# Kernel optimization log

Hardware: AMD Instinct MI355X
Metric: run time of the kernel (lower is better)

The kernel has to match this reference:

```python
import jax, jax.numpy as jnp
import numpy as np

N_VOXELS = 128
N_PARAMS = 8
N_QUERIES = 4194304


def setup_inputs() -> dict:
    key = jax.random.key(0)
    k1, k2 = jax.random.split(key)
    ipos = jax.random.uniform(k1, (N_QUERIES, 3), dtype=jnp.float32)  # positions in [0,1]^3
    grid = 0.01 * jax.random.normal(k2, (N_VOXELS, N_VOXELS, N_VOXELS, N_PARAMS), dtype=jnp.float32)
    return {"ipos": ipos, "grid": grid}


def reference(ipos, grid):
    # Trilinear interpolation lookup into a dense [V,V,V,P] voxel grid.
    V = grid.shape[0]
    p = jnp.clip(ipos, 0.0, 1.0) * (V - 1)          # [N,3] continuous grid coords
    i0 = jnp.clip(jnp.floor(p).astype(jnp.int32), 0, V - 2)  # [N,3] lower corner
    f = p - i0.astype(p.dtype)                        # [N,3] fractional offset
    i1 = i0 + 1
    x0, y0, z0 = i0[:, 0], i0[:, 1], i0[:, 2]
    x1, y1, z1 = i1[:, 0], i1[:, 1], i1[:, 2]
    fx, fy, fz = f[:, 0:1], f[:, 1:2], f[:, 2:3]      # keep [N,1] for broadcast over P
    gx, gy, gz = 1.0 - fx, 1.0 - fy, 1.0 - fz
    # 8 corner gathers, each [N,P]
    out = (grid[x0, y0, z0] * (gx * gy * gz)
         + grid[x0, y0, z1] * (gx * gy * fz)
         + grid[x0, y1, z0] * (gx * fy * gz)
         + grid[x0, y1, z1] * (gx * fy * fz)
         + grid[x1, y0, z0] * (fx * gy * gz)
         + grid[x1, y0, z1] * (fx * gy * fz)
         + grid[x1, y1, z0] * (fx * fy * gz)
         + grid[x1, y1, z1] * (fx * fy * fz))
    return out  # [N,P]
```

## Files before the change

### kernel.cpp

```cpp
#include <hip/hip_runtime.h>

#define NV 128
typedef unsigned int uint32;

#define TBL_ENTRIES ((size_t)NV * NV * NV)
#define TBL_BYTES   (TBL_ENTRIES * 64)

__global__ __launch_bounds__(256) void absmax_kernel(
        const float4* __restrict__ g4, float* __restrict__ M, int n4) {
    int tid = blockIdx.x * blockDim.x + threadIdx.x;
    int stride = gridDim.x * blockDim.x;
    float mm = 0.0f;
    for (int i = tid; i < n4; i += stride) {
        float4 v = g4[i];
        mm = fmaxf(mm, fmaxf(fmaxf(fabsf(v.x), fabsf(v.y)),
                             fmaxf(fabsf(v.z), fabsf(v.w))));
    }
    for (int off = 32; off > 0; off >>= 1)
        mm = fmaxf(mm, __shfl_down(mm, off));
    __shared__ float wm[4];
    int lane = threadIdx.x & 63, wv = threadIdx.x >> 6;
    if (lane == 0) wm[wv] = mm;
    __syncthreads();
    if (threadIdx.x == 0)
        M[blockIdx.x] = fmaxf(fmaxf(wm[0], wm[1]), fmaxf(wm[2], wm[3]));
}

__device__ __forceinline__ uint32 pack4(float4 v, float inv) {
    uint32 a = (uint32)__float2int_rn(v.x * inv) & 255u;
    uint32 b = (uint32)__float2int_rn(v.y * inv) & 255u;
    uint32 c = (uint32)__float2int_rn(v.z * inv) & 255u;
    uint32 d = (uint32)__float2int_rn(v.w * inv) & 255u;
    return a | (b << 8) | (c << 16) | (d << 24);
}

#define ROWSTRIDE 257

__global__ __launch_bounds__(256) void repack_full_kernel(
        const float* __restrict__ grid, const float* __restrict__ M,
        float* __restrict__ S, uint4* __restrict__ tbl) {
    __shared__ float4 lds4[10 * ROWSTRIDE];
    __shared__ float wm[4];
    int tid = threadIdx.x;
    int x  = blockIdx.x >> 5;
    int y0 = (blockIdx.x & 31) << 2;

    const float4* g4 = reinterpret_cast<const float4*>(grid);
    for (int i = tid; i < 10 * 256; i += 256) {
        int r = i >> 8, c = i & 255;
        int xi = r / 5, yj = r - xi * 5;
        int gx_ = min(x + xi, NV - 1);
        int gy_ = min(y0 + yj, NV - 1);
        lds4[r * ROWSTRIDE + c] = g4[(size_t)(gx_ * NV + gy_) * 256 + c];
    }

    const float4* M4 = reinterpret_cast<const float4*>(M);
    float4 mv = M4[tid];
    float mm = fmaxf(fmaxf(mv.x, mv.y), fmaxf(mv.z, mv.w));
    for (int off = 32; off > 0; off >>= 1)
        mm = fmaxf(mm, __shfl_down(mm, off));
    int lane = tid & 63, wv = tid >> 6;
    if (lane == 0) wm[wv] = mm;
    __syncthreads();
    float amax = fmaxf(fmaxf(wm[0], wm[1]), fmaxf(wm[2], wm[3]));
    if (blockIdx.x == 0 && tid == 0) *S = amax;
    float inv = 127.0f / amax;

    for (int i = tid; i < 2048; i += 256) {
        int L = i >> 2, w = i & 3;
        int z = L & 127, yy = L >> 7;
        int xr = w >> 1, yr = w & 1;
        int row = xr * 5 + yy + yr;
        int z1 = min(z + 1, NV - 1);
        float4 a0 = lds4[row * ROWSTRIDE + z * 2];
        float4 a1 = lds4[row * ROWSTRIDE + z * 2 + 1];
        float4 b0 = lds4[row * ROWSTRIDE + z1 * 2];
        float4 b1 = lds4[row * ROWSTRIDE + z1 * 2 + 1];
        uint4 word;
        word.x = pack4(a0, inv);
        word.y = pack4(a1, inv);
        word.z = pack4(b0, inv);
        word.w = pack4(b1, inv);
        size_t e = (size_t)((x * NV) + y0 + yy) * NV + z;
        tbl[e * 4 + w] = word;
    }
}

__device__ __forceinline__ float4 dec4(uint32 w) {
    return make_float4((float)((int)(w << 24) >> 24),
                       (float)((int)(w << 16) >> 24),
                       (float)((int)(w <<  8) >> 24),
                       (float)((int)  w       >> 24));
}

__device__ __forceinline__ void acc4(float4& a, float4 v, float w) {
    a.x = fmaf(v.x, w, a.x);
    a.y = fmaf(v.y, w, a.y);
    a.z = fmaf(v.z, w, a.z);
    a.w = fmaf(v.w, w, a.w);
}

__device__ __forceinline__ void cell_of(const float* pf, int slot,
                                        size_t& e, float& fx, float& fy, float& fz) {
    float px = pf[slot * 3 + 0];
    float py = pf[slot * 3 + 1];
    float pz = pf[slot * 3 + 2];
    px = fminf(fmaxf(px, 0.0f), 1.0f) * (float)(NV - 1);
    py = fminf(fmaxf(py, 0.0f), 1.0f) * (float)(NV - 1);
    pz = fminf(fmaxf(pz, 0.0f), 1.0f) * (float)(NV - 1);
    int x0 = min((int)px, NV - 2);
    int y0 = min((int)py, NV - 2);
    int z0 = min((int)pz, NV - 2);
    fx = px - (float)x0;
    fy = py - (float)y0;
    fz = pz - (float)z0;
    e = (size_t)((x0 * NV + y0) * NV + z0) * 4;
}

__device__ __forceinline__ void lerp_store(const uint4* E, float fx, float fy,
                                           float fz, float s, float4* o4, int q) {
    float gx = 1.0f - fx, gy = 1.0f - fy, gz = 1.0f - fz;
    float w0 = gx * gy, w1 = gx * fy, w2 = fx * gy, w3 = fx * fy;
    float4 a03 = make_float4(0.f, 0.f, 0.f, 0.f);
    float4 a47 = make_float4(0.f, 0.f, 0.f, 0.f);
    {
        float wg = w0 * gz, wf = w0 * fz;
        acc4(a03, dec4(E[0].x), wg); acc4(a47, dec4(E[0].y), wg);
        acc4(a03, dec4(E[0].z), wf); acc4(a47, dec4(E[0].w), wf);
    }
    {
        float wg = w1 * gz, wf = w1 * fz;
        acc4(a03, dec4(E[1].x), wg); acc4(a47, dec4(E[1].y), wg);
        acc4(a03, dec4(E[1].z), wf); acc4(a47, dec4(E[1].w), wf);
    }
    {
        float wg = w2 * gz, wf = w2 * fz;
        acc4(a03, dec4(E[2].x), wg); acc4(a47, dec4(E[2].y), wg);
        acc4(a03, dec4(E[2].z), wf); acc4(a47, dec4(E[2].w), wf);
    }
    {
        float wg = w3 * gz, wf = w3 * fz;
        acc4(a03, dec4(E[3].x), wg); acc4(a47, dec4(E[3].y), wg);
        acc4(a03, dec4(E[3].z), wf); acc4(a47, dec4(E[3].w), wf);
    }
    o4[q * 2 + 0] = make_float4(a03.x * s, a03.y * s, a03.z * s, a03.w * s);
    o4[q * 2 + 1] = make_float4(a47.x * s, a47.y * s, a47.z * s, a47.w * s);
}

__global__ __launch_bounds__(256) void trilerp_full_kernel(
        const float* __restrict__ ipos, const uint4* __restrict__ tbl,
        const float* __restrict__ S, float* __restrict__ out, int nq) {
    __shared__ float4 pls[384];
    int tid = threadIdx.x;
    int blk = blockIdx.x;
    const float4* ip4 = reinterpret_cast<const float4*>(ipos);
    int n4p = (int)(((long long)nq * 3) >> 2);
    int sbase = blk * 384;
    #pragma unroll
    for (int k = 0; k < 2; ++k) {
        int i = tid + k * 256;
        if (i < 384 && sbase + i < n4p) pls[i] = ip4[sbase + i];
    }
    __syncthreads();

    int q0 = blk * 512 + tid;
    int q1 = q0 + 256;
    const float* pf = reinterpret_cast<const float*>(pls);
    float s = (*S) * (1.0f / 127.0f);
    float4* o4 = reinterpret_cast<float4*>(out);

    size_t e0 = 0, e1 = 0;
    float fx0, fy0, fz0, fx1, fy1, fz1;
    bool v0 = q0 < nq, v1 = q1 < nq;
    if (v0) cell_of(pf, tid,       e0, fx0, fy0, fz0);
    if (v1) cell_of(pf, tid + 256, e1, fx1, fy1, fz1);

    uint4 E0[4], E1[4];
    if (v0) { E0[0] = tbl[e0]; E0[1] = tbl[e0+1]; E0[2] = tbl[e0+2]; E0[3] = tbl[e0+3]; }
    if (v1) { E1[0] = tbl[e1]; E1[1] = tbl[e1+1]; E1[2] = tbl[e1+2]; E1[3] = tbl[e1+3]; }

    if (v0) lerp_store(E0, fx0, fy0, fz0, s, o4, q0);
    if (v1) lerp_store(E1, fx1, fy1, fz1, s, o4, q1);
}

__device__ __forceinline__ float4 lerp4(float4 a, float4 b, float t) {
    return make_float4(fmaf(t, b.x - a.x, a.x),
                       fmaf(t, b.y - a.y, a.y),
                       fmaf(t, b.z - a.z, a.z),
                       fmaf(t, b.w - a.w, a.w));
}

__global__ __launch_bounds__(256) void voxel_trilerp_kernel(
        const float* __restrict__ ipos,
        const float* __restrict__ grid,
        float* __restrict__ out,
        int nq) {
    const int tid = blockIdx.x * blockDim.x + threadIdx.x;
    const int stride = gridDim.x * blockDim.x;
    const float4* __restrict__ g4 = reinterpret_cast<const float4*>(grid);
    float4* __restrict__ o4 = reinterpret_cast<float4*>(out);

    const int Z4 = 2;
    const int Y4 = NV * 8 / 4;
    const int X4 = NV * NV * 8 / 4;

    for (int q = tid; q < nq; q += stride) {
        float px = ipos[q * 3 + 0];
        float py = ipos[q * 3 + 1];
        float pz = ipos[q * 3 + 2];

        px = fminf(fmaxf(px, 0.0f), 1.0f) * (float)(NV - 1);
        py = fminf(fmaxf(py, 0.0f), 1.0f) * (float)(NV - 1);
        pz = fminf(fmaxf(pz, 0.0f), 1.0f) * (float)(NV - 1);

        int x0 = min((int)px, NV - 2);
        int y0 = min((int)py, NV - 2);
        int z0 = min((int)pz, NV - 2);

        float fx = px - (float)x0;
        float fy = py - (float)y0;
        float fz = pz - (float)z0;

        int b = x0 * X4 + y0 * Y4 + z0 * Z4;

        float4 c00a0 = g4[b],                c00a1 = g4[b + 1];
        float4 c00b0 = g4[b + Z4],           c00b1 = g4[b + Z4 + 1];
        float4 c01a0 = g4[b + Y4],           c01a1 = g4[b + Y4 + 1];
        float4 c01b0 = g4[b + Y4 + Z4],      c01b1 = g4[b + Y4 + Z4 + 1];
        float4 c10a0 = g4[b + X4],           c10a1 = g4[b + X4 + 1];
        float4 c10b0 = g4[b + X4 + Z4],      c10b1 = g4[b + X4 + Z4 + 1];
        float4 c11a0 = g4[b + X4 + Y4],      c11a1 = g4[b + X4 + Y4 + 1];
        float4 c11b0 = g4[b + X4 + Y4 + Z4], c11b1 = g4[b + X4 + Y4 + Z4 + 1];

        float4 z00_0 = lerp4(c00a0, c00b0, fz), z00_1 = lerp4(c00a1, c00b1, fz);
        float4 z01_0 = lerp4(c01a0, c01b0, fz), z01_1 = lerp4(c01a1, c01b1, fz);
        float4 z10_0 = lerp4(c10a0, c10b0, fz), z10_1 = lerp4(c10a1, c10b1, fz);
        float4 z11_0 = lerp4(c11a0, c11b0, fz), z11_1 = lerp4(c11a1, c11b1, fz);

        float4 y0_0 = lerp4(z00_0, z01_0, fy), y0_1 = lerp4(z00_1, z01_1, fy);
        float4 y1_0 = lerp4(z10_0, z11_0, fy), y1_1 = lerp4(z10_1, z11_1, fy);

        float4 r0 = lerp4(y0_0, y1_0, fx);
        float4 r1 = lerp4(y0_1, y1_1, fx);

        o4[q * 2 + 0] = r0;
        o4[q * 2 + 1] = r1;
    }
}

extern "C" void kernel_launch(void* const* d_in, const int* in_sizes, int n_in,
                              void* d_out, int out_size, void* d_ws, size_t ws_size,
                              hipStream_t stream) {
    const float* ipos = (const float*)d_in[0];
    const float* grid = (const float*)d_in[1];
    float* out = (float*)d_out;

    const int nq = in_sizes[0] / 3;
    const int ng4 = in_sizes[1] / 4;

    if (ws_size >= TBL_BYTES) {
        uint4* tbl = (uint4*)d_ws;
        float* M = (float*)((char*)d_ws + TBL_BYTES - 4096);
        float* S = (float*)((char*)d_ws + TBL_BYTES - 4096 - 64);

        absmax_kernel<<<1024, 256, 0, stream>>>(
            reinterpret_cast<const float4*>(grid), M, ng4);
        repack_full_kernel<<<127 * 32, 256, 0, stream>>>(grid, M, S, tbl);
        trilerp_full_kernel<<<(nq + 511) / 512, 256, 0, stream>>>(
            ipos, tbl, S, out, nq);
    } else {
        voxel_trilerp_kernel<<<2048, 256, 0, stream>>>(ipos, grid, out, nq);
    }
}
```

Measured before the change: 168.7 us.

## Fuse abs-max into repack with per-tile int8 scales, drop absmax pass

Removes the separate abs-max kernel that read the whole grid just to find one global scale. Each repack block now finds the max over the grid rows it already loads into shared memory, writes its own scale, and quantizes with it. The trilerp kernel looks up the matching per-tile scale for each query. This saves a full read of the grid and one kernel launch. In exchange there is one extra small, cached scale load per query and a change in quantization behaviour (per-tile rather than global scale).

```diff
diff --git a/kernel.cpp b/kernel.cpp
--- a/kernel.cpp
+++ b/kernel.cpp
@@ -6,25 +6,7 @@
 #define TBL_ENTRIES ((size_t)NV * NV * NV)
 #define TBL_BYTES   (TBL_ENTRIES * 64)
 
-__global__ __launch_bounds__(256) void absmax_kernel(
-        const float4* __restrict__ g4, float* __restrict__ M, int n4) {
-    int tid = blockIdx.x * blockDim.x + threadIdx.x;
-    int stride = gridDim.x * blockDim.x;
-    float mm = 0.0f;
-    for (int i = tid; i < n4; i += stride) {
-        float4 v = g4[i];
-        mm = fmaxf(mm, fmaxf(fmaxf(fabsf(v.x), fabsf(v.y)),
-                             fmaxf(fabsf(v.z), fabsf(v.w))));
-    }
-    for (int off = 32; off > 0; off >>= 1)
-        mm = fmaxf(mm, __shfl_down(mm, off));
-    __shared__ float wm[4];
-    int lane = threadIdx.x & 63, wv = threadIdx.x >> 6;
-    if (lane == 0) wm[wv] = mm;
-    __syncthreads();
-    if (threadIdx.x == 0)
-        M[blockIdx.x] = fmaxf(fmaxf(wm[0], wm[1]), fmaxf(wm[2], wm[3]));
-}
+#define ROWSTRIDE 257
 
 __device__ __forceinline__ uint32 pack4(float4 v, float inv) {
     uint32 a = (uint32)__float2int_rn(v.x * inv) & 255u;
@@ -34,11 +16,9 @@
     return a | (b << 8) | (c << 16) | (d << 24);
 }
 
-#define ROWSTRIDE 257
-
 __global__ __launch_bounds__(256) void repack_full_kernel(
-        const float* __restrict__ grid, const float* __restrict__ M,
-        float* __restrict__ S, uint4* __restrict__ tbl) {
+        const float* __restrict__ grid, float* __restrict__ Sc,
+        uint4* __restrict__ tbl) {
     __shared__ float4 lds4[10 * ROWSTRIDE];
     __shared__ float wm[4];
     int tid = threadIdx.x;
@@ -46,24 +26,25 @@
     int y0 = (blockIdx.x & 31) << 2;
 
     const float4* g4 = reinterpret_cast<const float4*>(grid);
+    float mm = 0.0f;
     for (int i = tid; i < 10 * 256; i += 256) {
         int r = i >> 8, c = i & 255;
         int xi = r / 5, yj = r - xi * 5;
         int gx_ = min(x + xi, NV - 1);
         int gy_ = min(y0 + yj, NV - 1);
-        lds4[r * ROWSTRIDE + c] = g4[(size_t)(gx_ * NV + gy_) * 256 + c];
-    }
-
-    const float4* M4 = reinterpret_cast<const float4*>(M);
-    float4 mv = M4[tid];
-    float mm = fmaxf(fmaxf(mv.x, mv.y), fmaxf(mv.z, mv.w));
+        float4 v = g4[(size_t)(gx_ * NV + gy_) * 256 + c];
+        lds4[r * ROWSTRIDE + c] = v;
+        mm = fmaxf(mm, fmaxf(fmaxf(fabsf(v.x), fabsf(v.y)),
+                             fmaxf(fabsf(v.z), fabsf(v.w))));
+    }
+
     for (int off = 32; off > 0; off >>= 1)
         mm = fmaxf(mm, __shfl_down(mm, off));
     int lane = tid & 63, wv = tid >> 6;
     if (lane == 0) wm[wv] = mm;
     __syncthreads();
-    float amax = fmaxf(fmaxf(wm[0], wm[1]), fmaxf(wm[2], wm[3]));
-    if (blockIdx.x == 0 && tid == 0) *S = amax;
+    float amax = fmaxf(fmaxf(fmaxf(wm[0], wm[1]), fmaxf(wm[2], wm[3])), 1e-30f);
+    if (tid == 0) Sc[blockIdx.x] = amax;
     float inv = 127.0f / amax;
 
     for (int i = tid; i < 2048; i += 256) {
@@ -100,8 +81,8 @@
     a.w = fmaf(v.w, w, a.w);
 }
 
-__device__ __forceinline__ void cell_of(const float* pf, int slot,
-                                        size_t& e, float& fx, float& fy, float& fz) {
+__device__ __forceinline__ void cell_of(const float* pf, int slot, size_t& e,
+                                        int& sidx, float& fx, float& fy, float& fz) {
     float px = pf[slot * 3 + 0];
     float py = pf[slot * 3 + 1];
     float pz = pf[slot * 3 + 2];
@@ -115,6 +96,7 @@
     fy = py - (float)y0;
     fz = pz - (float)z0;
     e = (size_t)((x0 * NV + y0) * NV + z0) * 4;
+    sidx = (x0 << 5) | (y0 >> 2);
 }
 
 __device__ __forceinline__ void lerp_store(const uint4* E, float fx, float fy,
@@ -149,7 +131,7 @@
 
 __global__ __launch_bounds__(256) void trilerp_full_kernel(
         const float* __restrict__ ipos, const uint4* __restrict__ tbl,
-        const float* __restrict__ S, float* __restrict__ out, int nq) {
+        const float* __restrict__ Sc, float* __restrict__ out, int nq) {
     __shared__ float4 pls[384];
     int tid = threadIdx.x;
     int blk = blockIdx.x;
@@ -166,21 +148,28 @@
     int q0 = blk * 512 + tid;
     int q1 = q0 + 256;
     const float* pf = reinterpret_cast<const float*>(pls);
-    float s = (*S) * (1.0f / 127.0f);
     float4* o4 = reinterpret_cast<float4*>(out);
 
     size_t e0 = 0, e1 = 0;
+    int si0 = 0, si1 = 0;
     float fx0, fy0, fz0, fx1, fy1, fz1;
     bool v0 = q0 < nq, v1 = q1 < nq;
-    if (v0) cell_of(pf, tid,       e0, fx0, fy0, fz0);
-    if (v1) cell_of(pf, tid + 256, e1, fx1, fy1, fz1);
+    if (v0) cell_of(pf, tid,       e0, si0, fx0, fy0, fz0);
+    if (v1) cell_of(pf, tid + 256, e1, si1, fx1, fy1, fz1);
 
     uint4 E0[4], E1[4];
-    if (v0) { E0[0] = tbl[e0]; E0[1] = tbl[e0+1]; E0[2] = tbl[e0+2]; E0[3] = tbl[e0+3]; }
-    if (v1) { E1[0] = tbl[e1]; E1[1] = tbl[e1+1]; E1[2] = tbl[e1+2]; E1[3] = tbl[e1+3]; }
-
-    if (v0) lerp_store(E0, fx0, fy0, fz0, s, o4, q0);
-    if (v1) lerp_store(E1, fx1, fy1, fz1, s, o4, q1);
+    float s0 = 0.f, s1 = 0.f;
+    if (v0) {
+        E0[0] = tbl[e0]; E0[1] = tbl[e0+1]; E0[2] = tbl[e0+2]; E0[3] = tbl[e0+3];
+        s0 = Sc[si0] * (1.0f / 127.0f);
+    }
+    if (v1) {
+        E1[0] = tbl[e1]; E1[1] = tbl[e1+1]; E1[2] = tbl[e1+2]; E1[3] = tbl[e1+3];
+        s1 = Sc[si1] * (1.0f / 127.0f);
+    }
+
+    if (v0) lerp_store(E0, fx0, fy0, fz0, s0, o4, q0);
+    if (v1) lerp_store(E1, fx1, fy1, fz1, s1, o4, q1);
 }
 
 __device__ __forceinline__ float4 lerp4(float4 a, float4 b, float t) {
@@ -256,18 +245,14 @@
     float* out = (float*)d_out;
 
     const int nq = in_sizes[0] / 3;
-    const int ng4 = in_sizes[1] / 4;
 
     if (ws_size >= TBL_BYTES) {
         uint4* tbl = (uint4*)d_ws;
-        float* M = (float*)((char*)d_ws + TBL_BYTES - 4096);
-        float* S = (float*)((char*)d_ws + TBL_BYTES - 4096 - 64);
-
-        absmax_kernel<<<1024, 256, 0, stream>>>(
-            reinterpret_cast<const float4*>(grid), M, ng4);
-        repack_full_kernel<<<127 * 32, 256, 0, stream>>>(grid, M, S, tbl);
+        float* Sc = (float*)((char*)d_ws + TBL_BYTES - 32768);
+
+        repack_full_kernel<<<127 * 32, 256, 0, stream>>>(grid, Sc, tbl);
         trilerp_full_kernel<<<(nq + 511) / 512, 256, 0, stream>>>(
-            ipos, tbl, S, out, nq);
+            ipos, tbl, Sc, out, nq);
     } else {
         voxel_trilerp_kernel<<<2048, 256, 0, stream>>>(ipos, grid, out, nq);
     }
```

New measurement: 170.2 us. About the same (+0.9%).
